# Optimization experiments

Hardware: AMD Instinct MI355X
Metric: run time of the kernel (lower is better)

The kernel has to match this reference:

```python
import jax, jax.numpy as jnp
import numpy as np

D_MODEL = 768
D_STATE = 16
K_CONV = 4
BATCH = 2
SEQ = 2048


def setup_inputs() -> dict:
    key = jax.random.key(0)
    ks = jax.random.split(key, 16)
    dm, ds, K = D_MODEL, D_STATE, K_CONV
    s = 0.02
    inp = {
        "x": jax.random.normal(ks[0], (BATCH, SEQ, dm), dtype=jnp.float32),
        # linear weights stored (in, out); y = x @ W + b (equivalent to torch Linear)
        "Wi": jax.random.normal(ks[1], (dm, 2 * dm), dtype=jnp.float32) * s,
        "bi": jnp.zeros((2 * dm,), jnp.float32),
        "Wconv": jax.random.normal(ks[2], (dm, K), dtype=jnp.float32) * s,
        "bconv": jnp.zeros((dm,), jnp.float32),
        "Wdt": jax.random.normal(ks[3], (dm, dm), dtype=jnp.float32) * s,
        "bdt": jnp.zeros((dm,), jnp.float32),
        "WB": jax.random.normal(ks[4], (dm, dm * ds), dtype=jnp.float32) * s,
        "bB": jnp.zeros((dm * ds,), jnp.float32),
        "WC": jax.random.normal(ks[5], (dm, dm * ds), dtype=jnp.float32) * s,
        "bC": jnp.zeros((dm * ds,), jnp.float32),
        "A_log": jnp.zeros((dm, ds), jnp.float32),  # matches nn.Parameter(torch.zeros)
        "D": jnp.ones((dm,), jnp.float32),          # matches nn.Parameter(torch.ones)
        "Wo": jax.random.normal(ks[6], (dm, dm), dtype=jnp.float32) * s,
        "bo": jnp.zeros((dm,), jnp.float32),
    }
    return inp


def _forward(x, Wi, bi, Wconv, bconv, Wdt, bdt, WB, bB, WC, bC, A_log, D, Wo, bo):
    B, L, dm = x.shape
    ds = A_log.shape[1]
    K = Wconv.shape[1]

    uv = x @ Wi + bi                        # (B, L, 2*dm)
    u, v = uv[..., :dm], uv[..., dm:]

    # causal depthwise conv1d: torch pads K-1 both sides, keeps first L outputs
    u_pad = jnp.pad(u, ((0, 0), (K - 1, 0), (0, 0)))
    u_conv = bconv + sum(u_pad[:, k:k + L, :] * Wconv[:, k] for k in range(K))

    dt = jax.nn.softplus(u_conv @ Wdt + bdt)            # (B, L, dm)
    Bt = (u_conv @ WB + bB).reshape(B, L, dm, ds)       # (B, L, dm, ds)
    Ct = (u_conv @ WC + bC).reshape(B, L, dm, ds)
    A = -jnp.exp(A_log)                                  # (dm, ds)

    def step(s, inputs):
        dt_t, u_t, B_tt, C_tt = inputs                   # (B,dm), (B,dm), (B,dm,ds), (B,dm,ds)
        dt_e = dt_t[..., None]
        s = s * jnp.exp(dt_e * A) + dt_e * B_tt * u_t[..., None]
        y = jnp.sum(C_tt * s, axis=-1) + D * u_t         # (B, dm)
        return s, y

    s0 = jnp.zeros((B, dm, ds), x.dtype)
    xs = (dt.transpose(1, 0, 2), u_conv.transpose(1, 0, 2),
          Bt.transpose(1, 0, 2, 3), Ct.transpose(1, 0, 2, 3))
    _, ys = jax.lax.scan(step, s0, xs)                   # ys: (L, B, dm)
    y = ys.transpose(1, 0, 2)

    y = y * jax.nn.sigmoid(v)
    return y @ Wo + bo


def reference(x, Wi, bi, Wconv, bconv, Wdt, bdt, WB, bB, WC, bC, A_log, D, Wo, bo):
    return _forward(x, Wi, bi, Wconv, bconv, Wdt, bdt, WB, bB, WC, bC, A_log, D, Wo, bo)
```

## Files before the change

### kernel.cpp

```cpp
#include <hip/hip_runtime.h>

#define DM 768
#define DS 16
#define SEQ 2048
#define BATCH 2
#define MROWS (BATCH*SEQ)
#define N_UV (2*DM)
#define N_BC (DM*DS)
#define NGRP (BATCH*DM/4)
#define SUBMAX 32

typedef _Float16 half8 __attribute__((ext_vector_type(8)));
typedef float floatx4 __attribute__((ext_vector_type(4)));

static __device__ __forceinline__ unsigned short f2h(float f) {
  _Float16 h = (_Float16)f;
  return __builtin_bit_cast(unsigned short, h);
}
static __device__ __forceinline__ float h2f(unsigned short u) {
  return (float)__builtin_bit_cast(_Float16, u);
}
static __device__ __forceinline__ float softplus_f(float x) {
  return (x > 20.f) ? x : log1pf(__expf(x));
}
static __device__ __forceinline__ void async_cp16(const unsigned short* g,
                                                  unsigned short* l) {
  __builtin_amdgcn_global_load_lds(
      (const __attribute__((address_space(1))) void*)g,
      (__attribute__((address_space(3))) void*)l, 16, 0, 0);
}
static __device__ __forceinline__ float row_reduce16(float v) {
  int x;
  x = __builtin_amdgcn_update_dpp(0, __builtin_bit_cast(int, v), 0x128, 0xf, 0xf, true);
  v += __builtin_bit_cast(float, x);
  x = __builtin_amdgcn_update_dpp(0, __builtin_bit_cast(int, v), 0x124, 0xf, 0xf, true);
  v += __builtin_bit_cast(float, x);
  x = __builtin_amdgcn_update_dpp(0, __builtin_bit_cast(int, v), 0x122, 0xf, 0xf, true);
  v += __builtin_bit_cast(float, x);
  x = __builtin_amdgcn_update_dpp(0, __builtin_bit_cast(int, v), 0x121, 0xf, 0xf, true);
  v += __builtin_bit_cast(float, x);
  return v;
}

__global__ void convert_f2h(const float* __restrict__ in,
                            unsigned short* __restrict__ out, int n) {
  int i = (blockIdx.x * blockDim.x + threadIdx.x) * 4;
  if (i >= n) return;
  float4 f = *(const float4*)(in + i);
  ushort4 h;
  h.x = f2h(f.x); h.y = f2h(f.y); h.z = f2h(f.z); h.w = f2h(f.w);
  *(ushort4*)(out + i) = h;
}

__global__ void transpose_f2h(const float* __restrict__ W,
                              unsigned short* __restrict__ WT, int K, int N) {
  __shared__ float tile[32][33];
  int n0 = blockIdx.x * 32, k0 = blockIdx.y * 32;
  int tx = threadIdx.x, ty = threadIdx.y;
#pragma unroll
  for (int i = 0; i < 32; i += 8)
    tile[ty + i][tx] = W[(size_t)(k0 + ty + i) * N + (n0 + tx)];
  __syncthreads();
#pragma unroll
  for (int i = 0; i < 32; i += 8)
    WT[(size_t)(n0 + ty + i) * K + (k0 + tx)] = f2h(tile[tx][ty + i]);
}

template<int ACT, int OUTH>
__global__ __launch_bounds__(256)
void gemm_f16(const unsigned short* __restrict__ A,
              const unsigned short* __restrict__ BT0,
              const unsigned short* __restrict__ BT1,
              const float* __restrict__ bias0,
              const float* __restrict__ bias1,
              void* __restrict__ Cout0,
              void* __restrict__ Cout1,
              int M, int N, int K, int TCa, int bstride, int row0) {
  const unsigned short* BT = blockIdx.z ? BT1 : BT0;
  const float* bias = blockIdx.z ? bias1 : bias0;
  void* Cout = blockIdx.z ? Cout1 : Cout0;
  __shared__ __align__(16) unsigned short As[128 * 32];
  __shared__ __align__(16) unsigned short Bs[128 * 32];
  const int m0 = blockIdx.y * 128, n0 = blockIdx.x * 128;
  const int tid = threadIdx.x;
  const int lane = tid & 63, wave = tid >> 6;
  const int wm = (wave >> 1) * 64, wn = (wave & 1) * 64;
  const int l16 = lane & 15, quad = lane >> 4;
  const int sr = tid >> 2;
  const int sc = (((tid & 3) ^ ((tid >> 3) & 3)) ) * 8;
  const int pch = (quad ^ ((l16 >> 1) & 3)) * 8;

  floatx4 acc[4][4] = {};

  const int mA0 = m0 + sr, mA1 = m0 + sr + 64;
  const int gA0 = (mA0 / TCa) * bstride + row0 + (mA0 % TCa);
  const int gA1 = (mA1 / TCa) * bstride + row0 + (mA1 % TCa);
  const unsigned short* Arow0 = A + (size_t)gA0 * K + sc;
  const unsigned short* Arow1 = A + (size_t)gA1 * K + sc;
  const unsigned short* Brow0 = BT + (size_t)(n0 + sr) * K + sc;
  const unsigned short* Brow1 = BT + (size_t)(n0 + sr + 64) * K + sc;
  unsigned short* ldsA0 = As + (wave * 16) * 32;
  unsigned short* ldsA1 = As + (64 + wave * 16) * 32;
  unsigned short* ldsB0 = Bs + (wave * 16) * 32;
  unsigned short* ldsB1 = Bs + (64 + wave * 16) * 32;

  for (int k0 = 0; k0 < K; k0 += 32) {
    async_cp16(Arow0 + k0, ldsA0);
    async_cp16(Arow1 + k0, ldsA1);
    async_cp16(Brow0 + k0, ldsB0);
    async_cp16(Brow1 + k0, ldsB1);
    __syncthreads();
    half8 af[4], bf[4];
#pragma unroll
    for (int i = 0; i < 4; i++) {
      af[i] = __builtin_bit_cast(half8, *(const uint4*)&As[(wm + i * 16 + l16) * 32 + pch]);
      bf[i] = __builtin_bit_cast(half8, *(const uint4*)&Bs[(wn + i * 16 + l16) * 32 + pch]);
    }
#pragma unroll
    for (int mi = 0; mi < 4; mi++)
#pragma unroll
      for (int ni = 0; ni < 4; ni++)
        acc[mi][ni] = __builtin_amdgcn_mfma_f32_16x16x32_f16(af[mi], bf[ni], acc[mi][ni], 0, 0, 0);
    __syncthreads();
  }

#pragma unroll
  for (int ni = 0; ni < 4; ni++) {
    int col = n0 + wn + ni * 16 + l16;
    float bv = bias[col];
#pragma unroll
    for (int mi = 0; mi < 4; mi++) {
#pragma unroll
      for (int r = 0; r < 4; r++) {
        int row = m0 + wm + mi * 16 + quad * 4 + r;
        float v = acc[mi][ni][r] + bv;
        if (ACT == 1) v = softplus_f(v);
        if (OUTH) ((unsigned short*)Cout)[(size_t)row * N + col] = f2h(v);
        else      ((float*)Cout)[(size_t)row * N + col] = v;
      }
    }
  }
}

__global__ void dwconv(const unsigned short* __restrict__ uv,
                       const float* __restrict__ Wconv,
                       const float* __restrict__ bconv,
                       unsigned short* __restrict__ uc) {
  int idx = blockIdx.x * 256 + threadIdx.x;
  int c = (idx % (DM / 2)) * 2;
  int row = idx / (DM / 2);
  int t = row & (SEQ - 1);
  float a0 = bconv[c], a1 = bconv[c + 1];
  const float* w0 = Wconv + c * 4;
  const float* w1 = Wconv + (c + 1) * 4;
#pragma unroll
  for (int k = 0; k < 4; k++) {
    int tt = t - 3 + k;
    if (tt >= 0) {
      ushort2 u2 = *(const ushort2*)&uv[(size_t)(row - 3 + k) * N_UV + c];
      a0 += h2f(u2.x) * w0[k];
      a1 += h2f(u2.y) * w1[k];
    }
  }
  ushort2 o; o.x = f2h(a0); o.y = f2h(a1);
  *(ushort2*)&uc[(size_t)row * DM + c] = o;
}

__global__ __launch_bounds__(64)
void scan_pass1(const unsigned short* __restrict__ dt,
                const unsigned short* __restrict__ uc,
                const unsigned short* __restrict__ Btc,
                const float* __restrict__ A_log,
                float* __restrict__ Ssub,
                float* __restrict__ Aexp,
                int ci, int TC, int SUBn) {
  const int TSUB = TC / SUBn;
  int wid = blockIdx.x, sub = blockIdx.y;
  int b = wid / (DM / 4);
  int c0 = (wid % (DM / 4)) * 4;
  int lane = threadIdx.x;
  int c = c0 + (lane >> 4);
  float Acj = -__expf(A_log[c0 * DS + lane]);
  int col = c0 * DS + lane;
  size_t gbase = (size_t)b * SEQ + (size_t)ci * TC + (size_t)sub * TSUB;
  size_t lbase = (size_t)b * TC + (size_t)sub * TSUB;

  float s = 0.f, dsum = 0.f;
  float n_dt[8], n_u[8], n_B[8];
#pragma unroll
  for (int i = 0; i < 8; i++) {
    n_dt[i] = h2f(dt[(gbase + i) * DM + c]);
    n_u[i]  = h2f(uc[(gbase + i) * DM + c]);
    n_B[i]  = h2f(Btc[(lbase + i) * N_BC + col]);
  }
  for (int t0 = 0; t0 < TSUB; t0 += 8) {
    float c_dt[8], c_u[8], c_B[8];
#pragma unroll
    for (int i = 0; i < 8; i++) { c_dt[i] = n_dt[i]; c_u[i] = n_u[i]; c_B[i] = n_B[i]; }
    if (t0 + 8 < TSUB) {
#pragma unroll
      for (int i = 0; i < 8; i++) {
        size_t gr = gbase + t0 + 8 + i, lr = lbase + t0 + 8 + i;
        n_dt[i] = h2f(dt[gr * DM + c]);
        n_u[i]  = h2f(uc[gr * DM + c]);
        n_B[i]  = h2f(Btc[lr * N_BC + col]);
      }
    }
#pragma unroll
    for (int i = 0; i < 8; i++) {
      float dtc = c_dt[i];
      dsum += dtc;
      float a = __expf(dtc * Acj);
      s = fmaf(s, a, dtc * c_B[i] * c_u[i]);
    }
  }
  int idx = (sub * BATCH + b) * N_BC + col;
  Ssub[idx] = s;
  Aexp[idx] = __expf(Acj * dsum);
}

__global__ __launch_bounds__(64)
void scan_combine(const float* __restrict__ Ssub, const float* __restrict__ Aexp,
                  float* __restrict__ Sinit, float* __restrict__ s_state,
                  int ci, int SUBn) {
  int wid = blockIdx.x;
  int b = wid / (DM / 4);
  int c0 = (wid % (DM / 4)) * 4;
  int col = c0 * DS + threadIdx.x;
  int sidx = b * N_BC + col;
  float s = (ci == 0) ? 0.f : s_state[sidx];
  for (int k = 0; k < SUBn; k++) {
    int idx = (k * BATCH + b) * N_BC + col;
    Sinit[idx] = s;
    s = fmaf(s, Aexp[idx], Ssub[idx]);
  }
  s_state[sidx] = s;
}

__global__ __launch_bounds__(64)
void scan_pass2(const unsigned short* __restrict__ dt,
                const unsigned short* __restrict__ uc,
                const unsigned short* __restrict__ Btc,
                const unsigned short* __restrict__ Ctc,
                const unsigned short* __restrict__ uv,
                const float* __restrict__ A_log,
                const float* __restrict__ Dv,
                const float* __restrict__ Sinit,
                unsigned short* __restrict__ yg,
                int ci, int TC, int SUBn) {
  const int TSUB = TC / SUBn;
  int wid = blockIdx.x, sub = blockIdx.y;
  int b = wid / (DM / 4);
  int c0 = (wid % (DM / 4)) * 4;
  int lane = threadIdx.x;
  int j = lane & 15;
  int c = c0 + (lane >> 4);
  float Acj = -__expf(A_log[c0 * DS + lane]);
  float Dc = Dv[c];
  int col = c0 * DS + lane;
  float s = Sinit[(sub * BATCH + b) * N_BC + col];
  size_t gbase = (size_t)b * SEQ + (size_t)ci * TC + (size_t)sub * TSUB;
  size_t lbase = (size_t)b * TC + (size_t)sub * TSUB;

  float n_dt[8], n_u[8], n_B[8], n_C[8], n_v[8];
#pragma unroll
  for (int i = 0; i < 8; i++) {
    size_t gr = gbase + i, lr = lbase + i;
    n_dt[i] = h2f(dt[gr * DM + c]);
    n_u[i]  = h2f(uc[gr * DM + c]);
    n_B[i]  = h2f(Btc[lr * N_BC + col]);
    n_C[i]  = h2f(Ctc[lr * N_BC + col]);
    n_v[i]  = h2f(uv[gr * N_UV + DM + c]);
  }
  for (int t0 = 0; t0 < TSUB; t0 += 8) {
    float c_dt[8], c_u[8], c_B[8], c_C[8], c_v[8];
#pragma unroll
    for (int i = 0; i < 8; i++) {
      c_dt[i] = n_dt[i]; c_u[i] = n_u[i]; c_B[i] = n_B[i];
      c_C[i] = n_C[i]; c_v[i] = n_v[i];
    }
    if (t0 + 8 < TSUB) {
#pragma unroll
      for (int i = 0; i < 8; i++) {
        size_t gr = gbase + t0 + 8 + i, lr = lbase + t0 + 8 + i;
        n_dt[i] = h2f(dt[gr * DM + c]);
        n_u[i]  = h2f(uc[gr * DM + c]);
        n_B[i]  = h2f(Btc[lr * N_BC + col]);
        n_C[i]  = h2f(Ctc[lr * N_BC + col]);
        n_v[i]  = h2f(uv[gr * N_UV + DM + c]);
      }
    }
#pragma unroll
    for (int i = 0; i < 8; i++) {
      float dtc = c_dt[i];
      float a = __expf(dtc * Acj);
      s = fmaf(s, a, dtc * c_B[i] * c_u[i]);
      float yt = row_reduce16(c_C[i] * s);
      if (j == 0) {
        float y = yt + Dc * c_u[i];
        float g = 1.f / (1.f + __expf(-c_v[i]));
        yg[(gbase + t0 + i) * DM + c] = f2h(y * g);
      }
    }
  }
}

extern "C" void kernel_launch(void* const* d_in, const int* in_sizes, int n_in,
                              void* d_out, int out_size, void* d_ws, size_t ws_size,
                              hipStream_t stream) {
  const float* x     = (const float*)d_in[0];
  const float* Wi    = (const float*)d_in[1];
  const float* bi    = (const float*)d_in[2];
  const float* Wconv = (const float*)d_in[3];
  const float* bconv = (const float*)d_in[4];
  const float* Wdt   = (const float*)d_in[5];
  const float* bdt   = (const float*)d_in[6];
  const float* WB    = (const float*)d_in[7];
  const float* bB    = (const float*)d_in[8];
  const float* WC    = (const float*)d_in[9];
  const float* bC    = (const float*)d_in[10];
  const float* A_log = (const float*)d_in[11];
  const float* Dv    = (const float*)d_in[12];
  const float* Wo    = (const float*)d_in[13];
  const float* bo    = (const float*)d_in[14];
  float* out = (float*)d_out;
  (void)in_sizes; (void)n_in; (void)out_size;

  auto pad = [](size_t b) { return (b + 255) & ~(size_t)255; };

  const size_t sz_xb   = pad((size_t)MROWS * DM * 2);
  const size_t sz_WiT  = pad((size_t)N_UV * DM * 2);
  const size_t sz_WdtT = pad((size_t)DM * DM * 2);
  const size_t sz_WBT  = pad((size_t)N_BC * DM * 2);
  const size_t sz_WCT  = pad((size_t)N_BC * DM * 2);
  const size_t sz_WoT  = pad((size_t)DM * DM * 2);
  const size_t sz_uvb  = pad((size_t)MROWS * N_UV * 2);
  const size_t sz_ucb  = pad((size_t)MROWS * DM * 2);
  const size_t sz_dtb  = pad((size_t)MROWS * DM * 2);
  const size_t sz_st   = pad((size_t)BATCH * N_BC * 4);
  const size_t sz_sub  = pad((size_t)SUBMAX * BATCH * N_BC * 4);
  const size_t fixed = sz_xb + sz_WiT + sz_WdtT + sz_WBT + sz_WCT + sz_WoT +
                       sz_uvb + sz_ucb + sz_dtb + sz_st + 3 * sz_sub;

  int NC = 16;
  for (int nc : {1, 2, 4, 8, 16}) {
    size_t need = fixed + 2 * pad((size_t)BATCH * (SEQ / nc) * N_BC * 2);
    if (need <= ws_size) { NC = nc; break; }
  }
  const int TC = SEQ / NC;
  const int MC = BATCH * TC;
  const int SUBn = (TC / 8 < SUBMAX) ? (TC / 8) : SUBMAX;

  char* ws = (char*)d_ws;
  size_t off = 0;
  auto alloc = [&](size_t bytes) { char* p = ws + off; off += bytes; return p; };
  unsigned short* xb   = (unsigned short*)alloc(sz_xb);
  unsigned short* WiT  = (unsigned short*)alloc(sz_WiT);
  unsigned short* WdtT = (unsigned short*)alloc(sz_WdtT);
  unsigned short* WBT  = (unsigned short*)alloc(sz_WBT);
  unsigned short* WCT  = (unsigned short*)alloc(sz_WCT);
  unsigned short* WoT  = (unsigned short*)alloc(sz_WoT);
  unsigned short* uvb  = (unsigned short*)alloc(sz_uvb);
  unsigned short* ucb  = (unsigned short*)alloc(sz_ucb);
  unsigned short* dtb  = (unsigned short*)alloc(sz_dtb);
  float*          sst  = (float*)alloc(sz_st);
  float*          Ssub = (float*)alloc(sz_sub);
  float*          Aexp = (float*)alloc(sz_sub);
  float*          Sini = (float*)alloc(sz_sub);
  unsigned short* Btc  = (unsigned short*)alloc(pad((size_t)MC * N_BC * 2));
  unsigned short* Ctc  = (unsigned short*)alloc(pad((size_t)MC * N_BC * 2));
  unsigned short* ygb  = xb;

  convert_f2h<<<dim3(MROWS * DM / 1024), dim3(256), 0, stream>>>(x, xb, MROWS * DM);
  transpose_f2h<<<dim3(N_UV / 32, DM / 32), dim3(32, 8), 0, stream>>>(Wi, WiT, DM, N_UV);
  transpose_f2h<<<dim3(DM / 32, DM / 32), dim3(32, 8), 0, stream>>>(Wdt, WdtT, DM, DM);
  transpose_f2h<<<dim3(N_BC / 32, DM / 32), dim3(32, 8), 0, stream>>>(WB, WBT, DM, N_BC);
  transpose_f2h<<<dim3(N_BC / 32, DM / 32), dim3(32, 8), 0, stream>>>(WC, WCT, DM, N_BC);
  transpose_f2h<<<dim3(DM / 32, DM / 32), dim3(32, 8), 0, stream>>>(Wo, WoT, DM, DM);

  gemm_f16<0, 1><<<dim3(N_UV / 128, MROWS / 128, 1), 256, 0, stream>>>(
      xb, WiT, WiT, bi, bi, uvb, uvb, MROWS, N_UV, DM, MROWS, 0, 0);
  dwconv<<<dim3(MROWS * DM / 512), 256, 0, stream>>>(uvb, Wconv, bconv, ucb);
  gemm_f16<1, 1><<<dim3(DM / 128, MROWS / 128, 1), 256, 0, stream>>>(
      ucb, WdtT, WdtT, bdt, bdt, dtb, dtb, MROWS, DM, DM, MROWS, 0, 0);

  for (int ci = 0; ci < NC; ci++) {
    gemm_f16<0, 1><<<dim3(N_BC / 128, MC / 128, 2), 256, 0, stream>>>(
        ucb, WBT, WCT, bB, bC, Btc, Ctc, MC, N_BC, DM, TC, SEQ, ci * TC);
    scan_pass1<<<dim3(NGRP, SUBn), 64, 0, stream>>>(dtb, ucb, Btc, A_log, Ssub, Aexp, ci, TC, SUBn);
    scan_combine<<<dim3(NGRP), 64, 0, stream>>>(Ssub, Aexp, Sini, sst, ci, SUBn);
    scan_pass2<<<dim3(NGRP, SUBn), 64, 0, stream>>>(dtb, ucb, Btc, Ctc, uvb,
                                                    A_log, Dv, Sini, ygb, ci, TC, SUBn);
  }

  gemm_f16<0, 0><<<dim3(DM / 128, MROWS / 128, 1), 256, 0, stream>>>(
      ygb, WoT, WoT, bo, bo, out, out, MROWS, DM, DM, MROWS, 0, 0);
}
```

Before: 626.8 us.

## Write dt/B/C GEMM outputs transposed so scan reads contiguous time vectors

Adds a TRANS epilogue to the f16 GEMM that stages the output tile through a swizzled LDS buffer and writes it column-major (channel-major, time contiguous). The dt and B/C projection GEMMs now use it, and both scan passes load 8 consecutive timesteps per lane with a single 16-byte vector load instead of 8 strided scalar loads. This is meant to cut the scan's scattered global memory traffic. The cost is extra LDS round trips and syncs in the GEMM epilogue.

After: 688.3 us. +9.8%, slower.

```diff
diff --git a/kernel.cpp b/kernel.cpp
--- a/kernel.cpp
+++ b/kernel.cpp
@@ -66,7 +66,7 @@
     WT[(size_t)(n0 + ty + i) * K + (k0 + tx)] = f2h(tile[tx][ty + i]);
 }
 
-template<int ACT, int OUTH>
+template<int ACT, int OUTH, int TRANS>
 __global__ __launch_bounds__(256)
 void gemm_f16(const unsigned short* __restrict__ A,
               const unsigned short* __restrict__ BT0,
@@ -75,19 +75,20 @@
               const float* __restrict__ bias1,
               void* __restrict__ Cout0,
               void* __restrict__ Cout1,
-              int M, int N, int K, int TCa, int bstride, int row0) {
+              int M, int N, int K, int TCa, int bstride, int row0, int ldT) {
   const unsigned short* BT = blockIdx.z ? BT1 : BT0;
   const float* bias = blockIdx.z ? bias1 : bias0;
   void* Cout = blockIdx.z ? Cout1 : Cout0;
-  __shared__ __align__(16) unsigned short As[128 * 32];
-  __shared__ __align__(16) unsigned short Bs[128 * 32];
+  __shared__ __align__(16) unsigned short smem[2 * 128 * 32];
+  unsigned short* As = smem;
+  unsigned short* Bs = smem + 128 * 32;
   const int m0 = blockIdx.y * 128, n0 = blockIdx.x * 128;
   const int tid = threadIdx.x;
   const int lane = tid & 63, wave = tid >> 6;
   const int wm = (wave >> 1) * 64, wn = (wave & 1) * 64;
   const int l16 = lane & 15, quad = lane >> 4;
   const int sr = tid >> 2;
-  const int sc = (((tid & 3) ^ ((tid >> 3) & 3)) ) * 8;
+  const int sc = (((tid & 3) ^ ((tid >> 3) & 3))) * 8;
   const int pch = (quad ^ ((l16 >> 1) & 3)) * 8;
 
   floatx4 acc[4][4] = {};
@@ -124,19 +125,56 @@
     __syncthreads();
   }
 
-#pragma unroll
-  for (int ni = 0; ni < 4; ni++) {
-    int col = n0 + wn + ni * 16 + l16;
-    float bv = bias[col];
-#pragma unroll
-    for (int mi = 0; mi < 4; mi++) {
-#pragma unroll
-      for (int r = 0; r < 4; r++) {
-        int row = m0 + wm + mi * 16 + quad * 4 + r;
-        float v = acc[mi][ni][r] + bv;
-        if (ACT == 1) v = softplus_f(v);
-        if (OUTH) ((unsigned short*)Cout)[(size_t)row * N + col] = f2h(v);
-        else      ((float*)Cout)[(size_t)row * N + col] = v;
+  if (TRANS) {
+#pragma unroll
+    for (int ph = 0; ph < 2; ph++) {
+      __syncthreads();
+#pragma unroll
+      for (int nn = 0; nn < 2; nn++) {
+        int ni = ph * 2 + nn;
+        int colb = wn + ni * 16 + l16;
+        int cc = (wn >> 1) + nn * 16 + l16;
+        float bv = bias[n0 + colb];
+#pragma unroll
+        for (int mi = 0; mi < 4; mi++) {
+          int slot = (wm >> 2) + mi * 4 + quad;
+          int pair = slot >> 1, bitb = slot & 1;
+          int phys = ((pair ^ (cc & 15)) << 1) | bitb;
+          union { _Float16 h[4]; unsigned long long u; } pk;
+#pragma unroll
+          for (int r = 0; r < 4; r++) {
+            float v = acc[mi][ni][r] + bv;
+            if (ACT == 1) v = softplus_f(v);
+            pk.h[r] = (_Float16)v;
+          }
+          *(unsigned long long*)&smem[cc * 128 + phys * 4] = pk.u;
+        }
+      }
+      __syncthreads();
+#pragma unroll
+      for (int pass = 0; pass < 4; pass++) {
+        int cc = (tid >> 4) + pass * 16;
+        int p16 = tid & 15;
+        uint4 v = *(const uint4*)&smem[cc * 128 + (p16 ^ (cc & 15)) * 8];
+        int colb = ((cc & 32) ? 64 : 0) + (ph * 2 + ((cc >> 4) & 1)) * 16 + (cc & 15);
+        *(uint4*)&((unsigned short*)Cout)[(size_t)(n0 + colb) * ldT + m0 + p16 * 8] = v;
+      }
+    }
+  } else {
+#pragma unroll
+    for (int ni = 0; ni < 4; ni++) {
+      int col = n0 + wn + ni * 16 + l16;
+      float bv = bias[col];
+#pragma unroll
+      for (int mi = 0; mi < 4; mi++) {
+#pragma unroll
+        for (int r = 0; r < 4; r++) {
+          int row = m0 + wm + mi * 16 + quad * 4 + r;
+          float v = acc[mi][ni][r] + bv;
+          if (ACT == 1) v = softplus_f(v);
+          if (OUTH) ((unsigned short*)Cout)[(size_t)row * N + col] = f2h(v);
+          else      ((float*)Cout)[(size_t)row * N + col] = v;
+        }
       }
     }
   }
@@ -167,14 +205,15 @@
 }
 
 __global__ __launch_bounds__(64)
-void scan_pass1(const unsigned short* __restrict__ dt,
+void scan_pass1(const unsigned short* __restrict__ dtT,
                 const unsigned short* __restrict__ uc,
-                const unsigned short* __restrict__ Btc,
+                const unsigned short* __restrict__ BtcT,
                 const float* __restrict__ A_log,
                 float* __restrict__ Ssub,
                 float* __restrict__ Aexp,
                 int ci, int TC, int SUBn) {
   const int TSUB = TC / SUBn;
+  const int MC = BATCH * TC;
   int wid = blockIdx.x, sub = blockIdx.y;
   int b = wid / (DM / 4);
   int c0 = (wid % (DM / 4)) * 4;
@@ -184,34 +223,34 @@
   int col = c0 * DS + lane;
   size_t gbase = (size_t)b * SEQ + (size_t)ci * TC + (size_t)sub * TSUB;
   size_t lbase = (size_t)b * TC + (size_t)sub * TSUB;
+  const unsigned short* pB = BtcT + (size_t)col * MC + lbase;
+  const unsigned short* pD = dtT + (size_t)c * MROWS + gbase;
 
   float s = 0.f, dsum = 0.f;
-  float n_dt[8], n_u[8], n_B[8];
-#pragma unroll
-  for (int i = 0; i < 8; i++) {
-    n_dt[i] = h2f(dt[(gbase + i) * DM + c]);
-    n_u[i]  = h2f(uc[(gbase + i) * DM + c]);
-    n_B[i]  = h2f(Btc[(lbase + i) * N_BC + col]);
-  }
+  uint4 vB = *(const uint4*)pB;
+  uint4 vD = *(const uint4*)pD;
+  float n_u[8];
+#pragma unroll
+  for (int i = 0; i < 8; i++) n_u[i] = h2f(uc[(gbase + i) * DM + c]);
+
   for (int t0 = 0; t0 < TSUB; t0 += 8) {
-    float c_dt[8], c_u[8], c_B[8];
-#pragma unroll
-    for (int i = 0; i < 8; i++) { c_dt[i] = n_dt[i]; c_u[i] = n_u[i]; c_B[i] = n_B[i]; }
+    half8 hB = __builtin_bit_cast(half8, vB);
+    half8 hD = __builtin_bit_cast(half8, vD);
+    float c_u[8];
+#pragma unroll
+    for (int i = 0; i < 8; i++) c_u[i] = n_u[i];
     if (t0 + 8 < TSUB) {
-#pragma unroll
-      for (int i = 0; i < 8; i++) {
-        size_t gr = gbase + t0 + 8 + i, lr = lbase + t0 + 8 + i;
-        n_dt[i] = h2f(dt[gr * DM + c]);
-        n_u[i]  = h2f(uc[gr * DM + c]);
-        n_B[i]  = h2f(Btc[lr * N_BC + col]);
-      }
+      vB = *(const uint4*)(pB + t0 + 8);
+      vD = *(const uint4*)(pD + t0 + 8);
+#pragma unroll
+      for (int i = 0; i < 8; i++) n_u[i] = h2f(uc[(gbase + t0 + 8 + i) * DM + c]);
     }
 #pragma unroll
     for (int i = 0; i < 8; i++) {
-      float dtc = c_dt[i];
+      float dtc = (float)hD[i];
       dsum += dtc;
       float a = __expf(dtc * Acj);
-      s = fmaf(s, a, dtc * c_B[i] * c_u[i]);
+      s = fmaf(s, a, dtc * (float)hB[i] * c_u[i]);
     }
   }
   int idx = (sub * BATCH + b) * N_BC + col;
@@ -238,10 +277,10 @@
 }
 
 __global__ __launch_bounds__(64)
-void scan_pass2(const unsigned short* __restrict__ dt,
+void scan_pass2(const unsigned short* __restrict__ dtT,
                 const unsigned short* __restrict__ uc,
-                const unsigned short* __restrict__ Btc,
-                const unsigned short* __restrict__ Ctc,
+                const unsigned short* __restrict__ BtcT,
+                const unsigned short* __restrict__ CtcT,
                 const unsigned short* __restrict__ uv,
                 const float* __restrict__ A_log,
                 const float* __restrict__ Dv,
@@ -249,6 +288,7 @@
                 unsigned short* __restrict__ yg,
                 int ci, int TC, int SUBn) {
   const int TSUB = TC / SUBn;
+  const int MC = BATCH * TC;
   int wid = blockIdx.x, sub = blockIdx.y;
   int b = wid / (DM / 4);
   int c0 = (wid % (DM / 4)) * 4;
@@ -261,41 +301,43 @@
   float s = Sinit[(sub * BATCH + b) * N_BC + col];
   size_t gbase = (size_t)b * SEQ + (size_t)ci * TC + (size_t)sub * TSUB;
   size_t lbase = (size_t)b * TC + (size_t)sub * TSUB;
-
-  float n_dt[8], n_u[8], n_B[8], n_C[8], n_v[8];
+  const unsigned short* pB = BtcT + (size_t)col * MC + lbase;
+  const unsigned short* pC = CtcT + (size_t)col * MC + lbase;
+  const unsigned short* pD = dtT + (size_t)c * MROWS + gbase;
+
+  uint4 vB = *(const uint4*)pB;
+  uint4 vC = *(const uint4*)pC;
+  uint4 vD = *(const uint4*)pD;
+  float n_u[8], n_v[8];
 #pragma unroll
   for (int i = 0; i < 8; i++) {
-    size_t gr = gbase + i, lr = lbase + i;
-    n_dt[i] = h2f(dt[gr * DM + c]);
-    n_u[i]  = h2f(uc[gr * DM + c]);
-    n_B[i]  = h2f(Btc[lr * N_BC + col]);
-    n_C[i]  = h2f(Ctc[lr * N_BC + col]);
-    n_v[i]  = h2f(uv[gr * N_UV + DM + c]);
-  }
+    n_u[i] = h2f(uc[(gbase + i) * DM + c]);
+    n_v[i] = h2f(uv[(gbase + i) * N_UV + DM + c]);
+  }
+
   for (int t0 = 0; t0 < TSUB; t0 += 8) {
-    float c_dt[8], c_u[8], c_B[8], c_C[8], c_v[8];
+    half8 hB = __builtin_bit_cast(half8, vB);
+    half8 hC = __builtin_bit_cast(half8, vC);
+    half8 hD = __builtin_bit_cast(half8, vD);
+    float c_u[8], c_v[8];
+#pragma unroll
+    for (int i = 0; i < 8; i++) { c_u[i] = n_u[i]; c_v[i] = n_v[i]; }
+    if (t0 + 8 < TSUB) {
+      vB = *(const uint4*)(pB + t0 + 8);
+      vC = *(const uint4*)(pC + t0 + 8);
+      vD = *(const uint4*)(pD + t0 + 8);
+#pragma unroll
+      for (int i = 0; i < 8; i++) {
+        n_u[i] = h2f(uc[(gbase + t0 + 8 + i) * DM + c]);
+        n_v[i] = h2f(uv[(gbase + t0 + 8 + i) * N_UV + DM + c]);
+      }
+    }
 #pragma unroll
     for (int i = 0; i < 8; i++) {
-      c_dt[i] = n_dt[i]; c_u[i] = n_u[i]; c_B[i] = n_B[i];
-      c_C[i] = n_C[i]; c_v[i] = n_v[i];
-    }
-    if (t0 + 8 < TSUB) {
-#pragma unroll
-      for (int i = 0; i < 8; i++) {
-        size_t gr = gbase + t0 + 8 + i, lr = lbase + t0 + 8 + i;
-        n_dt[i] = h2f(dt[gr * DM + c]);
-        n_u[i]  = h2f(uc[gr * DM + c]);
-        n_B[i]  = h2f(Btc[lr * N_BC + col]);
-        n_C[i]  = h2f(Ctc[lr * N_BC + col]);
-        n_v[i]  = h2f(uv[gr * N_UV + DM + c]);
-      }
-    }
-#pragma unroll
-    for (int i = 0; i < 8; i++) {
-      float dtc = c_dt[i];
+      float dtc = (float)hD[i];
       float a = __expf(dtc * Acj);
-      s = fmaf(s, a, dtc * c_B[i] * c_u[i]);
-      float yt = row_reduce16(c_C[i] * s);
+      s = fmaf(s, a, dtc * (float)hB[i] * c_u[i]);
+      float yt = row_reduce16((float)hC[i] * s);
       if (j == 0) {
         float y = yt + Dc * c_u[i];
         float g = 1.f / (1.f + __expf(-c_v[i]));
@@ -378,21 +420,21 @@
   transpose_f2h<<<dim3(N_BC / 32, DM / 32), dim3(32, 8), 0, stream>>>(WC, WCT, DM, N_BC);
   transpose_f2h<<<dim3(DM / 32, DM / 32), dim3(32, 8), 0, stream>>>(Wo, WoT, DM, DM);
 
-  gemm_f16<0, 1><<<dim3(N_UV / 128, MROWS / 128, 1), 256, 0, stream>>>(
-      xb, WiT, WiT, bi, bi, uvb, uvb, MROWS, N_UV, DM, MROWS, 0, 0);
+  gemm_f16<0, 1, 0><<<dim3(N_UV / 128, MROWS / 128, 1), 256, 0, stream>>>(
+      xb, WiT, WiT, bi, bi, uvb, uvb, MROWS, N_UV, DM, MROWS, 0, 0, 0);
   dwconv<<<dim3(MROWS * DM / 512), 256, 0, stream>>>(uvb, Wconv, bconv, ucb);
-  gemm_f16<1, 1><<<dim3(DM / 128, MROWS / 128, 1), 256, 0, stream>>>(
-      ucb, WdtT, WdtT, bdt, bdt, dtb, dtb, MROWS, DM, DM, MROWS, 0, 0);
+  gemm_f16<1, 1, 1><<<dim3(DM / 128, MROWS / 128, 1), 256, 0, stream>>>(
+      ucb, WdtT, WdtT, bdt, bdt, dtb, dtb, MROWS, DM, DM, MROWS, 0, 0, MROWS);
 
   for (int ci = 0; ci < NC; ci++) {
-    gemm_f16<0, 1><<<dim3(N_BC / 128, MC / 128, 2), 256, 0, stream>>>(
-        ucb, WBT, WCT, bB, bC, Btc, Ctc, MC, N_BC, DM, TC, SEQ, ci * TC);
+    gemm_f16<0, 1, 1><<<dim3(N_BC / 128, MC / 128, 2), 256, 0, stream>>>(
+        ucb, WBT, WCT, bB, bC, Btc, Ctc, MC, N_BC, DM, TC, SEQ, ci * TC, MC);
     scan_pass1<<<dim3(NGRP, SUBn), 64, 0, stream>>>(dtb, ucb, Btc, A_log, Ssub, Aexp, ci, TC, SUBn);
     scan_combine<<<dim3(NGRP), 64, 0, stream>>>(Ssub, Aexp, Sini, sst, ci, SUBn);
     scan_pass2<<<dim3(NGRP, SUBn), 64, 0, stream>>>(dtb, ucb, Btc, Ctc, uvb,
                                                     A_log, Dv, Sini, ygb, ci, TC, SUBn);
   }
 
-  gemm_f16<0, 0><<<dim3(DM / 128, MROWS / 128, 1), 256, 0, stream>>>(
-      ygb, WoT, WoT, bo, bo, out, out, MROWS, DM, DM, MROWS, 0, 0);
-}
+  gemm_f16<0, 0, 0><<<dim3(DM / 128, MROWS / 128, 1), 256, 0, stream>>>(
+      ygb, WoT, WoT, bo, bo, out, out, MROWS, DM, DM, MROWS, 0, 0, 0);
+}
```

## Raise scan sub-chunk count, fuse weight transposes, alias Sinit onto Ssub

Applied to the files above, without the earlier changes.

Doubles the maximum number of scan sub-chunks so pass1 and pass2 launch more blocks per chunk, giving the sequential scan more parallelism. The combine kernel is templated on the sub-chunk count and preloads all partial states into registers before writing Sinit in place over Ssub, which frees one workspace buffer. The five weight transposes are merged into one launch that writes packed half2 values. The extra buffer headroom may allow fewer chunks (NC), and higher SUBn raises register use in combine.

Result: faster. 599.6 us (-4.4%).

```diff
diff --git a/kernel.cpp b/kernel.cpp
--- a/kernel.cpp
+++ b/kernel.cpp
@@ -8,7 +8,7 @@
 #define N_UV (2*DM)
 #define N_BC (DM*DS)
 #define NGRP (BATCH*DM/4)
-#define SUBMAX 32
+#define SUBMAX 64
 
 typedef _Float16 half8 __attribute__((ext_vector_type(8)));
 typedef float floatx4 __attribute__((ext_vector_type(4)));
@@ -52,18 +52,38 @@
   *(ushort4*)(out + i) = h;
 }
 
-__global__ void transpose_f2h(const float* __restrict__ W,
-                              unsigned short* __restrict__ WT, int K, int N) {
+__global__ void transpose_w5(const float* __restrict__ W0, const float* __restrict__ W1,
+                             const float* __restrict__ W2, const float* __restrict__ W3,
+                             const float* __restrict__ W4,
+                             unsigned short* __restrict__ T0, unsigned short* __restrict__ T1,
+                             unsigned short* __restrict__ T2, unsigned short* __restrict__ T3,
+                             unsigned short* __restrict__ T4,
+                             int N0, int N1, int N2, int N3, int N4) {
+  const float* W; unsigned short* WT; int N;
+  switch (blockIdx.z) {
+    case 0: W = W0; WT = T0; N = N0; break;
+    case 1: W = W1; WT = T1; N = N1; break;
+    case 2: W = W2; WT = T2; N = N2; break;
+    case 3: W = W3; WT = T3; N = N3; break;
+    default: W = W4; WT = T4; N = N4; break;
+  }
+  int n0 = blockIdx.x * 32;
+  if (n0 >= N) return;
+  int k0 = blockIdx.y * 32;
   __shared__ float tile[32][33];
-  int n0 = blockIdx.x * 32, k0 = blockIdx.y * 32;
   int tx = threadIdx.x, ty = threadIdx.y;
 #pragma unroll
   for (int i = 0; i < 32; i += 8)
     tile[ty + i][tx] = W[(size_t)(k0 + ty + i) * N + (n0 + tx)];
   __syncthreads();
-#pragma unroll
-  for (int i = 0; i < 32; i += 8)
-    WT[(size_t)(n0 + ty + i) * K + (k0 + tx)] = f2h(tile[tx][ty + i]);
+  int kp = tx & 15, half = tx >> 4;
+#pragma unroll
+  for (int i = 0; i < 2; i++) {
+    int nl = ty + half * 8 + i * 16;
+    unsigned int pk = (unsigned int)f2h(tile[2 * kp][nl]) |
+                      ((unsigned int)f2h(tile[2 * kp + 1][nl]) << 16);
+    *(unsigned int*)&WT[(size_t)(n0 + nl) * DM + k0 + 2 * kp] = pk;
+  }
 }
 
 template<int ACT, int OUTH>
@@ -87,7 +107,7 @@
   const int wm = (wave >> 1) * 64, wn = (wave & 1) * 64;
   const int l16 = lane & 15, quad = lane >> 4;
   const int sr = tid >> 2;
-  const int sc = (((tid & 3) ^ ((tid >> 3) & 3)) ) * 8;
+  const int sc = (((tid & 3) ^ ((tid >> 3) & 3))) * 8;
   const int pch = (quad ^ ((l16 >> 1) & 3)) * 8;
 
   floatx4 acc[4][4] = {};
@@ -219,20 +239,28 @@
   Aexp[idx] = __expf(Acj * dsum);
 }
 
+template<int SUBN>
 __global__ __launch_bounds__(64)
-void scan_combine(const float* __restrict__ Ssub, const float* __restrict__ Aexp,
-                  float* __restrict__ Sinit, float* __restrict__ s_state,
-                  int ci, int SUBn) {
+void scan_combine(const float* Ssub, const float* Aexp,
+                  float* Sinit, float* s_state, int ci) {
   int wid = blockIdx.x;
   int b = wid / (DM / 4);
   int c0 = (wid % (DM / 4)) * 4;
   int col = c0 * DS + threadIdx.x;
   int sidx = b * N_BC + col;
+  float sa[SUBN], ae[SUBN];
+#pragma unroll
+  for (int k = 0; k < SUBN; k++) {
+    int idx = (k * BATCH + b) * N_BC + col;
+    sa[k] = Ssub[idx];
+    ae[k] = Aexp[idx];
+  }
   float s = (ci == 0) ? 0.f : s_state[sidx];
-  for (int k = 0; k < SUBn; k++) {
+#pragma unroll
+  for (int k = 0; k < SUBN; k++) {
     int idx = (k * BATCH + b) * N_BC + col;
     Sinit[idx] = s;
-    s = fmaf(s, Aexp[idx], Ssub[idx]);
+    s = fmaf(s, ae[k], sa[k]);
   }
   s_state[sidx] = s;
 }
@@ -340,7 +368,7 @@
   const size_t sz_st   = pad((size_t)BATCH * N_BC * 4);
   const size_t sz_sub  = pad((size_t)SUBMAX * BATCH * N_BC * 4);
   const size_t fixed = sz_xb + sz_WiT + sz_WdtT + sz_WBT + sz_WCT + sz_WoT +
-                       sz_uvb + sz_ucb + sz_dtb + sz_st + 3 * sz_sub;
+                       sz_uvb + sz_ucb + sz_dtb + sz_st + 2 * sz_sub;
 
   int NC = 16;
   for (int nc : {1, 2, 4, 8, 16}) {
@@ -366,17 +394,14 @@
   float*          sst  = (float*)alloc(sz_st);
   float*          Ssub = (float*)alloc(sz_sub);
   float*          Aexp = (float*)alloc(sz_sub);
-  float*          Sini = (float*)alloc(sz_sub);
   unsigned short* Btc  = (unsigned short*)alloc(pad((size_t)MC * N_BC * 2));
   unsigned short* Ctc  = (unsigned short*)alloc(pad((size_t)MC * N_BC * 2));
   unsigned short* ygb  = xb;
+  float*          Sini = Ssub;
 
   convert_f2h<<<dim3(MROWS * DM / 1024), dim3(256), 0, stream>>>(x, xb, MROWS * DM);
-  transpose_f2h<<<dim3(N_UV / 32, DM / 32), dim3(32, 8), 0, stream>>>(Wi, WiT, DM, N_UV);
-  transpose_f2h<<<dim3(DM / 32, DM / 32), dim3(32, 8), 0, stream>>>(Wdt, WdtT, DM, DM);
-  transpose_f2h<<<dim3(N_BC / 32, DM / 32), dim3(32, 8), 0, stream>>>(WB, WBT, DM, N_BC);
-  transpose_f2h<<<dim3(N_BC / 32, DM / 32), dim3(32, 8), 0, stream>>>(WC, WCT, DM, N_BC);
-  transpose_f2h<<<dim3(DM / 32, DM / 32), dim3(32, 8), 0, stream>>>(Wo, WoT, DM, DM);
+  transpose_w5<<<dim3(N_BC / 32, DM / 32, 5), dim3(32, 8), 0, stream>>>(
+      Wi, Wdt, WB, WC, Wo, WiT, WdtT, WBT, WCT, WoT, N_UV, DM, N_BC, N_BC, DM);
 
   gemm_f16<0, 1><<<dim3(N_UV / 128, MROWS / 128, 1), 256, 0, stream>>>(
       xb, WiT, WiT, bi, bi, uvb, uvb, MROWS, N_UV, DM, MROWS, 0, 0);
@@ -387,8 +412,13 @@
   for (int ci = 0; ci < NC; ci++) {
     gemm_f16<0, 1><<<dim3(N_BC / 128, MC / 128, 2), 256, 0, stream>>>(
         ucb, WBT, WCT, bB, bC, Btc, Ctc, MC, N_BC, DM, TC, SEQ, ci * TC);
-    scan_pass1<<<dim3(NGRP, SUBn), 64, 0, stream>>>(dtb, ucb, Btc, A_log, Ssub, Aexp, ci, TC, SUBn);
-    scan_combine<<<dim3(NGRP), 64, 0, stream>>>(Ssub, Aexp, Sini, sst, ci, SUBn);
+    scan_pass1<<<dim3(NGRP, SUBn), 64, 0, stream>>>(dtb, ucb, Btc, A_log,
+                                                    Ssub, Aexp, ci, TC, SUBn);
+    switch (SUBn) {
+      case 64: scan_combine<64><<<dim3(NGRP), 64, 0, stream>>>(Ssub, Aexp, Sini, sst, ci); break;
+      case 32: scan_combine<32><<<dim3(NGRP), 64, 0, stream>>>(Ssub, Aexp, Sini, sst, ci); break;
+      default: scan_combine<16><<<dim3(NGRP), 64, 0, stream>>>(Ssub, Aexp, Sini, sst, ci); break;
+    }
     scan_pass2<<<dim3(NGRP, SUBn), 64, 0, stream>>>(dtb, ucb, Btc, Ctc, uvb,
                                                     A_log, Dv, Sini, ygb, ci, TC, SUBn);
   }
```
